# Performance work log

Measured on AMD Instinct MI355X. Metric: run time of the kernel, lower is better.

The kernel has to match this reference:

```python
import jax, jax.numpy as jnp
import numpy as np

MAX_SIZE = 650   # hard-coded node count in the original module
HIDDEN = 512     # hidden_dim
BATCH = 512      # batch_size (conv4 out channels)
IN_DIM = 512
N_EDGES = 150000


def _segment_softmax(e, dst, n):
    # torch_geometric.utils.softmax over destination-node segments
    m = jax.ops.segment_max(e, dst, num_segments=n)
    ex = jnp.exp(e - m[dst])
    s = jax.ops.segment_sum(ex, dst, num_segments=n)
    return ex / (s[dst] + 1e-16)


def _gat_conv(x, src, dst, W, a_src, a_dst, b, n, neg_slope=0.2):
    # PyG GATConv, heads=1, edge_dim=None (edge_attr ignored)
    h = x @ W                            # [n, out]
    al_s = h @ a_src                     # [n] per-node source attention logit
    al_d = h @ a_dst                     # [n] per-node dest attention logit
    e = jax.nn.leaky_relu(al_s[src] + al_d[dst], neg_slope)   # [E]
    alpha = _segment_softmax(e, dst, n)                        # [E]
    out = jax.ops.segment_sum(alpha[:, None] * h[src], dst, num_segments=n)
    return out + b


def setup_inputs() -> dict:
    key = jax.random.key(0)
    ks = jax.random.split(key, 12)
    inp = {
        "x_s": jax.random.normal(ks[0], (400, IN_DIM), jnp.float32),
        "x_t": jax.random.normal(ks[1], (250, IN_DIM), jnp.float32),
        "edge_index": jax.random.randint(ks[2], (2, N_EDGES), 0, MAX_SIZE, dtype=jnp.int32),
        "distances": jax.random.uniform(ks[3], (N_EDGES,), jnp.float32),
        "batch": jnp.zeros((MAX_SIZE,), jnp.int32),
        "W1": jax.random.normal(ks[4], (IN_DIM, HIDDEN), jnp.float32) / np.sqrt(IN_DIM).astype(np.float32),
        "a_src1": jax.random.normal(ks[5], (HIDDEN,), jnp.float32) * 0.1,
        "a_dst1": jax.random.normal(ks[6], (HIDDEN,), jnp.float32) * 0.1,
        "b1": jnp.zeros((HIDDEN,), jnp.float32),
        "W4": jax.random.normal(ks[7], (HIDDEN, BATCH), jnp.float32) / np.sqrt(HIDDEN).astype(np.float32),
        "a_src4": jax.random.normal(ks[8], (BATCH,), jnp.float32) * 0.1,
        "a_dst4": jax.random.normal(ks[9], (BATCH,), jnp.float32) * 0.1,
        "b4": jnp.zeros((BATCH,), jnp.float32),
        "fc_w": jax.random.normal(ks[10], (1, MAX_SIZE), jnp.float32) / np.sqrt(MAX_SIZE).astype(np.float32),
        "fc_b": jnp.zeros((1,), jnp.float32),
    }
    return inp


def reference(x_s, x_t, edge_index, distances, batch,
              W1, a_src1, a_dst1, b1, W4, a_src4, a_dst4, b4, fc_w, fc_b):
    # distances (edge_attr) and batch are unpacked but unused, as in the
    # original (GATConv with edge_dim=None ignores edge_attr).
    x = jnp.concatenate([x_s, x_t], axis=0)
    pad_n = max(MAX_SIZE - x.shape[0], 0)
    x = jnp.pad(x, ((0, pad_n), (0, 0)))            # [650, IN_DIM]
    # add_self_loops=True (PyG GATConv default)
    loop = jnp.arange(MAX_SIZE, dtype=edge_index.dtype)
    src = jnp.concatenate([edge_index[0], loop])
    dst = jnp.concatenate([edge_index[1], loop])
    x = _gat_conv(x, src, dst, W1, a_src1, a_dst1, b1, MAX_SIZE)
    x = jax.nn.relu(x)
    x = _gat_conv(x, src, dst, W4, a_src4, a_dst4, b4, MAX_SIZE)
    x = jax.nn.leaky_relu(x, 0.01)                  # [650, BATCH]
    x = x.reshape(BATCH, MAX_SIZE)                  # torch .view semantics (no transpose)
    x = x @ fc_w.T + fc_b                           # [BATCH, 1]
    x = x.squeeze()[None, :]                        # [1, BATCH]
    return jax.nn.sigmoid(x)
```

## Files before the change

### kernel.cpp

```cpp
#include <hip/hip_runtime.h>
#include <math.h>

#define N_NODES 650
#define DIM     512
#define E_RAW   150000
#define E_TOT   150650
#define WK      672
#define ZF      8
#define ZA      6
#define RSP     656

__global__ __launch_bounds__(256)
void k_feat(const float* __restrict__ A, const float* __restrict__ Axt,
            const float* __restrict__ B,
            const float* __restrict__ asrc, const float* __restrict__ adst,
            const float* __restrict__ Qin, const float* __restrict__ rspp,
            const float* __restrict__ bp,
            float* __restrict__ P, float* __restrict__ alsp, float* __restrict__ aldp,
            int a_mode) {
    __shared__ float Ast[16][68];
    __shared__ float Bs[16][64];
    int t = threadIdx.x;
    int tx4 = (t & 15) * 4, ty4 = (t >> 4) * 4;
    int row0 = blockIdx.y * 64, col0 = blockIdx.x * 64;
    int z = blockIdx.z;
    int kbase = z * 64;
    int ar = t >> 2, ak = (t & 3) * 4;
    int bk = t >> 4, bn = (t & 15) * 4;
    float acc[4][4] = {};
    int gr_a = row0 + ar;

    float inv = 0.f;
    if (a_mode == 3 && gr_a < N_NODES) {
        float r = 0.f;
        #pragma unroll
        for (int zz = 0; zz < ZA; zz++) r += rspp[zz * RSP + gr_a];
        inv = 1.f / (r + 1e-16f);
    }

    for (int kb = kbase; kb < kbase + 64; kb += 16) {
        {
            float4 v = make_float4(0.f, 0.f, 0.f, 0.f);
            if (gr_a < N_NODES) {
                if (a_mode == 1) {
                    const float* rowp = (gr_a < 400) ? A + (size_t)gr_a * DIM
                                                     : Axt + (size_t)(gr_a - 400) * DIM;
                    v = *(const float4*)(rowp + kb + ak);
                } else {
                    size_t rb = (size_t)gr_a * ZA * DIM + kb + ak;
                    float4 q = *(const float4*)(Qin + rb);
                    #pragma unroll
                    for (int zz = 1; zz < ZA; zz++) {
                        float4 q2 = *(const float4*)(Qin + rb + (size_t)zz * DIM);
                        q.x += q2.x; q.y += q2.y; q.z += q2.z; q.w += q2.w;
                    }
                    float4 bb = *(const float4*)&bp[kb + ak];
                    v.x = fmaxf(fmaf(q.x, inv, bb.x), 0.f);
                    v.y = fmaxf(fmaf(q.y, inv, bb.y), 0.f);
                    v.z = fmaxf(fmaf(q.z, inv, bb.z), 0.f);
                    v.w = fmaxf(fmaf(q.w, inv, bb.w), 0.f);
                }
            }
            Ast[ak + 0][ar] = v.x; Ast[ak + 1][ar] = v.y;
            Ast[ak + 2][ar] = v.z; Ast[ak + 3][ar] = v.w;
        }
        *(float4*)&Bs[bk][bn] = *(const float4*)&B[(size_t)(kb + bk) * DIM + col0 + bn];
        __syncthreads();
        #pragma unroll
        for (int kk = 0; kk < 16; kk++) {
            float4 a = *(const float4*)&Ast[kk][ty4];
            float4 b = *(const float4*)&Bs[kk][tx4];
            acc[0][0] += a.x*b.x; acc[0][1] += a.x*b.y; acc[0][2] += a.x*b.z; acc[0][3] += a.x*b.w;
            acc[1][0] += a.y*b.x; acc[1][1] += a.y*b.y; acc[1][2] += a.y*b.z; acc[1][3] += a.y*b.w;
            acc[2][0] += a.z*b.x; acc[2][1] += a.z*b.y; acc[2][2] += a.z*b.z; acc[2][3] += a.z*b.w;
            acc[3][0] += a.w*b.x; acc[3][1] += a.w*b.y; acc[3][2] += a.w*b.z; acc[3][3] += a.w*b.w;
        }
        __syncthreads();
    }

    float4 as4 = *(const float4*)&asrc[col0 + tx4];
    float4 ad4 = *(const float4*)&adst[col0 + tx4];
    int slice = z * 8 + blockIdx.x;
    #pragma unroll
    for (int i = 0; i < 4; i++) {
        int gr = row0 + ty4 + i;
        float sa = acc[i][0]*as4.x + acc[i][1]*as4.y + acc[i][2]*as4.z + acc[i][3]*as4.w;
        float sd = acc[i][0]*ad4.x + acc[i][1]*ad4.y + acc[i][2]*ad4.z + acc[i][3]*ad4.w;
        #pragma unroll
        for (int o = 8; o > 0; o >>= 1) {
            sa += __shfl_down(sa, o, 16);
            sd += __shfl_down(sd, o, 16);
        }
        if (gr < N_NODES) {
            *(float4*)&P[((size_t)gr * ZF + z) * DIM + col0 + tx4] =
                make_float4(acc[i][0], acc[i][1], acc[i][2], acc[i][3]);
            if ((t & 15) == 0) {
                alsp[gr * 64 + slice] = sa;
                aldp[gr * 64 + slice] = sd;
            }
        }
    }
}

__global__ __launch_bounds__(256)
void k_build(const int* __restrict__ ei,
             const float* __restrict__ alsp, const float* __restrict__ aldp,
             float* __restrict__ W) {
    __shared__ float als[N_NODES], ald[N_NODES];
    int t = threadIdx.x;
    for (int l = t; l < N_NODES; l += 256) {
        const float4* ap = (const float4*)(alsp + l * 64);
        const float4* dp = (const float4*)(aldp + l * 64);
        float sa = 0.f, sd = 0.f;
        #pragma unroll
        for (int j = 0; j < 16; j++) {
            float4 a = ap[j]; sa += a.x + a.y + a.z + a.w;
            float4 d = dp[j]; sd += d.x + d.y + d.z + d.w;
        }
        als[l] = sa; ald[l] = sd;
    }
    __syncthreads();
    const int stride = gridDim.x * 256;
    for (int i = blockIdx.x * 256 + t; i < E_TOT; i += stride) {
        int s, d;
        if (i < E_RAW) { s = ei[i]; d = ei[E_RAW + i]; }
        else           { s = d = i - E_RAW; }
        float e = als[s] + ald[d];
        e = e > 0.f ? e : 0.2f * e;
        atomicAdd(&W[(size_t)d * WK + s], __expf(e));
    }
}

__global__ __launch_bounds__(256)
void k_agg(const float* __restrict__ W, const float* __restrict__ P,
           float* __restrict__ Q, float* __restrict__ rsp) {
    __shared__ float Ast[16][68];
    __shared__ float Bs[16][64];
    int t = threadIdx.x;
    int tx4 = (t & 15) * 4, ty4 = (t >> 4) * 4;
    int row0 = blockIdx.y * 64, col0 = blockIdx.x * 64;
    int kbase = blockIdx.z * 112;
    int ar = t >> 2, ak = (t & 3) * 4;
    int bk = t >> 4, bn = (t & 15) * 4;
    float acc[4][4] = {};
    float rowSum = 0.f;
    int gr_a = row0 + ar;

    for (int kb = kbase; kb < kbase + 112; kb += 16) {
        {
            float4 v = make_float4(0.f, 0.f, 0.f, 0.f);
            if (gr_a < N_NODES)
                v = *(const float4*)(W + (size_t)gr_a * WK + kb + ak);
            rowSum += v.x + v.y + v.z + v.w;
            Ast[ak + 0][ar] = v.x; Ast[ak + 1][ar] = v.y;
            Ast[ak + 2][ar] = v.z; Ast[ak + 3][ar] = v.w;
        }
        {
            size_t pb = (size_t)(kb + bk) * ZF * DIM + col0 + bn;
            float4 b = *(const float4*)(P + pb);
            #pragma unroll
            for (int zz = 1; zz < ZF; zz++) {
                float4 b2 = *(const float4*)(P + pb + (size_t)zz * DIM);
                b.x += b2.x; b.y += b2.y; b.z += b2.z; b.w += b2.w;
            }
            *(float4*)&Bs[bk][bn] = b;
        }
        __syncthreads();
        #pragma unroll
        for (int kk = 0; kk < 16; kk++) {
            float4 a = *(const float4*)&Ast[kk][ty4];
            float4 b = *(const float4*)&Bs[kk][tx4];
            acc[0][0] += a.x*b.x; acc[0][1] += a.x*b.y; acc[0][2] += a.x*b.z; acc[0][3] += a.x*b.w;
            acc[1][0] += a.y*b.x; acc[1][1] += a.y*b.y; acc[1][2] += a.y*b.z; acc[1][3] += a.y*b.w;
            acc[2][0] += a.z*b.x; acc[2][1] += a.z*b.y; acc[2][2] += a.z*b.z; acc[2][3] += a.z*b.w;
            acc[3][0] += a.w*b.x; acc[3][1] += a.w*b.y; acc[3][2] += a.w*b.z; acc[3][3] += a.w*b.w;
        }
        __syncthreads();
    }

    rowSum += __shfl_xor(rowSum, 1);
    rowSum += __shfl_xor(rowSum, 2);
    if (blockIdx.x == 0 && (t & 3) == 0 && gr_a < N_NODES)
        rsp[blockIdx.z * RSP + gr_a] = rowSum;

    #pragma unroll
    for (int i = 0; i < 4; i++) {
        int gr = row0 + ty4 + i;
        if (gr < N_NODES)
            *(float4*)&Q[((size_t)gr * ZA + blockIdx.z) * DIM + col0 + tx4] =
                make_float4(acc[i][0], acc[i][1], acc[i][2], acc[i][3]);
    }
}

__global__ void k_final(const float* __restrict__ Q, const float* __restrict__ rsp,
                        const float* __restrict__ bias,
                        const float* __restrict__ fcw, const float* __restrict__ fcb,
                        float* __restrict__ out) {
    int b = blockIdx.x * 4 + (threadIdx.x >> 6);
    int lane = threadIdx.x & 63;
    if (b >= 512) return;
    float s = 0.f;
    for (int i = lane; i < N_NODES; i += 64) {
        int j = b * N_NODES + i;
        int r = j >> 9, c = j & 511;
        float q = 0.f, rsum = 0.f;
        #pragma unroll
        for (int zz = 0; zz < ZA; zz++) {
            q    += Q[((size_t)r * ZA + zz) * DIM + c];
            rsum += rsp[zz * RSP + r];
        }
        float v = fmaf(q, 1.f / (rsum + 1e-16f), bias[c]);
        v = v > 0.f ? v : 0.01f * v;
        s += v * fcw[i];
    }
    #pragma unroll
    for (int o = 32; o > 0; o >>= 1) s += __shfl_down(s, o);
    if (lane == 0) out[b] = 1.f / (1.f + expf(-(s + fcb[0])));
}

extern "C" void kernel_launch(void* const* d_in, const int* in_sizes, int n_in,
                              void* d_out, int out_size, void* d_ws, size_t ws_size,
                              hipStream_t stream) {
    const float* x_s   = (const float*)d_in[0];
    const float* x_t   = (const float*)d_in[1];
    const int*   ei    = (const int*)d_in[2];
    const float* W1    = (const float*)d_in[5];
    const float* asrc1 = (const float*)d_in[6];
    const float* adst1 = (const float*)d_in[7];
    const float* b1    = (const float*)d_in[8];
    const float* W4    = (const float*)d_in[9];
    const float* asrc4 = (const float*)d_in[10];
    const float* adst4 = (const float*)d_in[11];
    const float* b4    = (const float*)d_in[12];
    const float* fcw   = (const float*)d_in[13];
    const float* fcb   = (const float*)d_in[14];
    float* out = (float*)d_out;

    float* ws   = (float*)d_ws;
    float* P    = ws;
    float* W1d  = P + (size_t)WK * ZF * DIM;
    float* W2d  = W1d + (size_t)N_NODES * WK;
    float* Q    = W2d + (size_t)N_NODES * WK;
    float* alsp = Q + (size_t)N_NODES * ZA * DIM;
    float* aldp = alsp + N_NODES * 64;
    float* rsp1 = aldp + N_NODES * 64;
    float* rsp2 = rsp1 + ZA * RSP;

    float* zbeg = P + (size_t)N_NODES * ZF * DIM;
    size_t zbytes = (size_t)((WK - N_NODES) * ZF * DIM
                           + 2 * N_NODES * WK)
                    * sizeof(float);
    hipMemsetAsync(zbeg, 0, zbytes, stream);

    dim3 gF(DIM / 64, (N_NODES + 63) / 64, ZF);
    dim3 gA(DIM / 64, (N_NODES + 63) / 64, ZA);

    k_feat<<<gF, 256, 0, stream>>>(x_s, x_t, W1, asrc1, adst1,
                                   nullptr, nullptr, nullptr, P, alsp, aldp, 1);
    k_build<<<128, 256, 0, stream>>>(ei, alsp, aldp, W1d);
    k_agg<<<gA, 256, 0, stream>>>(W1d, P, Q, rsp1);

    k_feat<<<gF, 256, 0, stream>>>(nullptr, nullptr, W4, asrc4, adst4,
                                   Q, rsp1, b1, P, alsp, aldp, 3);
    k_build<<<128, 256, 0, stream>>>(ei, alsp, aldp, W2d);
    k_agg<<<gA, 256, 0, stream>>>(W2d, P, Q, rsp2);

    k_final<<<128, 256, 0, stream>>>(Q, rsp2, b4, fcw, fcb, out);
}
```

Before: 188.9 us.

## Fold memset into feature kernel and pre-reduce split-K partials in build kernel

```diff
diff --git a/kernel.cpp b/kernel.cpp
--- a/kernel.cpp
+++ b/kernel.cpp
@@ -10,6 +10,9 @@
 #define ZA      6
 #define RSP     656
 
+#define NZ4     ((22 * ZF * DIM + 2 * N_NODES * WK) / 4)
+#define Z4PB    343
+
 __global__ __launch_bounds__(256)
 void k_feat(const float* __restrict__ A, const float* __restrict__ Axt,
             const float* __restrict__ B,
@@ -17,7 +20,7 @@
             const float* __restrict__ Qin, const float* __restrict__ rspp,
             const float* __restrict__ bp,
             float* __restrict__ P, float* __restrict__ alsp, float* __restrict__ aldp,
-            int a_mode) {
+            float* __restrict__ zbase, int a_mode) {
     __shared__ float Ast[16][68];
     __shared__ float Bs[16][64];
     int t = threadIdx.x;
@@ -100,14 +103,25 @@
             }
         }
     }
+
+    if (a_mode == 1) {
+        int bid = blockIdx.x + 8 * blockIdx.y + 88 * blockIdx.z;
+        float4* z4 = (float4*)zbase;
+        int s0 = bid * Z4PB;
+        int s1 = s0 + Z4PB < NZ4 ? s0 + Z4PB : NZ4;
+        for (int i = s0 + t; i < s1; i += 256)
+            z4[i] = make_float4(0.f, 0.f, 0.f, 0.f);
+    }
 }
 
 __global__ __launch_bounds__(256)
 void k_build(const int* __restrict__ ei,
              const float* __restrict__ alsp, const float* __restrict__ aldp,
+             const float* __restrict__ P, float* __restrict__ hbuf,
              float* __restrict__ W) {
     __shared__ float als[N_NODES], ald[N_NODES];
     int t = threadIdx.x;
+    const int stride = gridDim.x * 256;
     for (int l = t; l < N_NODES; l += 256) {
         const float4* ap = (const float4*)(alsp + l * 64);
         const float4* dp = (const float4*)(aldp + l * 64);
@@ -120,7 +134,6 @@
         als[l] = sa; ald[l] = sd;
     }
     __syncthreads();
-    const int stride = gridDim.x * 256;
     for (int i = blockIdx.x * 256 + t; i < E_TOT; i += stride) {
         int s, d;
         if (i < E_RAW) { s = ei[i]; d = ei[E_RAW + i]; }
@@ -129,10 +142,24 @@
         e = e > 0.f ? e : 0.2f * e;
         atomicAdd(&W[(size_t)d * WK + s], __expf(e));
     }
+    const int n4 = WK * DIM / 4;
+    const float4* P4 = (const float4*)P;
+    float4* h4 = (float4*)hbuf;
+    for (int i = blockIdx.x * 256 + t; i < n4; i += stride) {
+        int kk = i >> 7, c4 = i & 127;
+        const float4* pb = P4 + ((size_t)kk * ZF) * 128 + c4;
+        float4 a = pb[0];
+        #pragma unroll
+        for (int zz = 1; zz < ZF; zz++) {
+            float4 b = pb[zz * 128];
+            a.x += b.x; a.y += b.y; a.z += b.z; a.w += b.w;
+        }
+        h4[i] = a;
+    }
 }
 
 __global__ __launch_bounds__(256)
-void k_agg(const float* __restrict__ W, const float* __restrict__ P,
+void k_agg(const float* __restrict__ W, const float* __restrict__ hbuf,
            float* __restrict__ Q, float* __restrict__ rsp) {
     __shared__ float Ast[16][68];
     __shared__ float Bs[16][64];
@@ -155,16 +182,7 @@
             Ast[ak + 0][ar] = v.x; Ast[ak + 1][ar] = v.y;
             Ast[ak + 2][ar] = v.z; Ast[ak + 3][ar] = v.w;
         }
-        {
-            size_t pb = (size_t)(kb + bk) * ZF * DIM + col0 + bn;
-            float4 b = *(const float4*)(P + pb);
-            #pragma unroll
-            for (int zz = 1; zz < ZF; zz++) {
-                float4 b2 = *(const float4*)(P + pb + (size_t)zz * DIM);
-                b.x += b2.x; b.y += b2.y; b.z += b2.z; b.w += b2.w;
-            }
-            *(float4*)&Bs[bk][bn] = b;
-        }
+        *(float4*)&Bs[bk][bn] = *(const float4*)&hbuf[(size_t)(kb + bk) * DIM + col0 + bn];
         __syncthreads();
         #pragma unroll
         for (int kk = 0; kk < 16; kk++) {
@@ -240,30 +258,28 @@
     float* P    = ws;
     float* W1d  = P + (size_t)WK * ZF * DIM;
     float* W2d  = W1d + (size_t)N_NODES * WK;
-    float* Q    = W2d + (size_t)N_NODES * WK;
+    float* hbuf = W2d + (size_t)N_NODES * WK;
+    float* Q    = hbuf + (size_t)WK * DIM;
     float* alsp = Q + (size_t)N_NODES * ZA * DIM;
     float* aldp = alsp + N_NODES * 64;
     float* rsp1 = aldp + N_NODES * 64;
     float* rsp2 = rsp1 + ZA * RSP;
 
-    float* zbeg = P + (size_t)N_NODES * ZF * DIM;
-    size_t zbytes = (size_t)((WK - N_NODES) * ZF * DIM
-                           + 2 * N_NODES * WK)
-                    * sizeof(float);
-    hipMemsetAsync(zbeg, 0, zbytes, stream);
+    float* zbase = P + (size_t)N_NODES * ZF * DIM;
 
     dim3 gF(DIM / 64, (N_NODES + 63) / 64, ZF);
     dim3 gA(DIM / 64, (N_NODES + 63) / 64, ZA);
 
     k_feat<<<gF, 256, 0, stream>>>(x_s, x_t, W1, asrc1, adst1,
-                                   nullptr, nullptr, nullptr, P, alsp, aldp, 1);
-    k_build<<<128, 256, 0, stream>>>(ei, alsp, aldp, W1d);
-    k_agg<<<gA, 256, 0, stream>>>(W1d, P, Q, rsp1);
+                                   nullptr, nullptr, nullptr,
+                                   P, alsp, aldp, zbase, 1);
+    k_build<<<512, 256, 0, stream>>>(ei, alsp, aldp, P, hbuf, W1d);
+    k_agg<<<gA, 256, 0, stream>>>(W1d, hbuf, Q, rsp1);
 
     k_feat<<<gF, 256, 0, stream>>>(nullptr, nullptr, W4, asrc4, adst4,
-                                   Q, rsp1, b1, P, alsp, aldp, 3);
-    k_build<<<128, 256, 0, stream>>>(ei, alsp, aldp, W2d);
-    k_agg<<<gA, 256, 0, stream>>>(W2d, P, Q, rsp2);
+                                   Q, rsp1, b1, P, alsp, aldp, zbase, 3);
+    k_build<<<512, 256, 0, stream>>>(ei, alsp, aldp, P, hbuf, W2d);
+    k_agg<<<gA, 256, 0, stream>>>(W2d, hbuf, Q, rsp2);
 
     k_final<<<128, 256, 0, stream>>>(Q, rsp2, b4, fcw, fcb, out);
 }
```

Measured after the change: 202.7 us. 1.07x slower.
